# Optimization experiments

Measured on AMD Instinct MI355X. Metric: run time of the kernel, lower is better.

The kernel has to match this reference:

```python
import jax, jax.numpy as jnp
import numpy as np

N, T, F, ND, D = 64, 96, 32, 8, 128


def setup_inputs() -> dict:
    key = jax.random.key(0)
    ks = jax.random.split(key, 12)
    x = jax.random.normal(ks[0], (N, T, F), jnp.float32)
    # Wq/Wk/Wv are an (N_dim,T,D) base tiled F times -> (F*N_dim, T, D)
    Wq = jnp.tile(jax.random.normal(ks[1], (ND, T, D), jnp.float32), (F, 1, 1))
    Wk = jnp.tile(jax.random.normal(ks[2], (ND, T, D), jnp.float32), (F, 1, 1))
    Wv = jnp.tile(jax.random.normal(ks[3], (ND, T, D), jnp.float32), (F, 1, 1))
    bq = jnp.zeros((F * ND, 1, D), jnp.float32)
    bk = jnp.zeros((F * ND, 1, D), jnp.float32)
    bv = jnp.zeros((F * ND, 1, D), jnp.float32)
    # torch nn.Linear weights are (out, in); kaiming fan_in std = sqrt(2/fan_in)
    fan1 = ND * N * N
    w1 = jax.random.normal(ks[4], (ND, fan1), jnp.float32) * np.sqrt(2.0 / fan1)
    b1 = jax.random.uniform(ks[5], (ND,), jnp.float32, -0.01, 0.01)
    w2 = jax.random.normal(ks[6], (1, ND), jnp.float32) * np.sqrt(2.0 / ND)
    b2 = jax.random.uniform(ks[7], (1,), jnp.float32, -0.01, 0.01)
    w3 = jax.random.normal(ks[8], (D, D * ND), jnp.float32) * np.sqrt(2.0 / (D * ND))
    b3 = jax.random.uniform(ks[9], (D,), jnp.float32, -0.01, 0.01)
    w4 = jax.random.normal(ks[10], (T, D), jnp.float32) * np.sqrt(2.0 / D)
    b4 = jax.random.uniform(ks[11], (T,), jnp.float32, -0.01, 0.01)
    return {"x": x, "Wq": Wq, "Wk": Wk, "Wv": Wv, "bq": bq, "bk": bk, "bv": bv,
            "w1": w1, "b1": b1, "w2": w2, "b2": b2, "w3": w3, "b3": b3,
            "w4": w4, "b4": b4, "N_dim": ND}


def reference(x, Wq, Wk, Wv, bq, bk, bv, w1, b1, w2, b2, w3, b3, w4, b4, N_dim):
    n, t, f = x.shape
    d = Wq.shape[2]
    nd = N_dim
    xp = jnp.transpose(x, (2, 0, 1))                       # (F, N, T)
    # expand over heads and flatten to batched matmul: (F*N_dim, N, T)
    mat_a = jnp.broadcast_to(xp[:, None, :, :], (f, nd, n, t)).reshape(f * nd, n, t)
    q = jnp.einsum('bnt,btd->bnd', mat_a, Wq) + bq         # (F*ND, N, D)
    k = jnp.einsum('bnt,btd->bnd', mat_a, Wk) + bk
    v = jnp.einsum('bnt,btd->bnd', mat_a, Wv) + bv
    q_ = q.reshape(f, nd, n, d)
    k_ = k.reshape(f, nd, n, d)
    v_ = v.reshape(f, nd, n, d)
    # pairwise feature-feature QK^T without materializing the expanded copies
    alpha = jnp.einsum('fknd,gkmd->fgknm', q_, k_) * (d ** -0.5)  # (F,F,ND,N,N)
    alpha = alpha.reshape(f, f, nd * n * n)
    # dropout layers are identity in eval mode
    h = jax.nn.relu(alpha @ w1.T + b1)                     # (F, F, ND)
    logits = (h @ w2.T + b2)[..., 0]                       # (F, F)
    att_score = jax.nn.softmax(logits, axis=1)
    b = jnp.einsum('ij,jklm->iklm', att_score, v_)         # (F, ND, N, D)
    b = jnp.transpose(b, (0, 2, 3, 1)).reshape(f, n, d * nd)
    y = jax.nn.relu(b @ w3.T + b3)                         # (F, N, D)
    y = y @ w4.T + b4                                      # (F, N, T)
    return jnp.transpose(y, (1, 2, 0)), att_score          # (N, T, F), (F, F)
```

## Files before the change

### kernel.cpp

```cpp
#include <hip/hip_runtime.h>

#define SQKD 0.08838834764831845f

typedef __attribute__((ext_vector_type(8))) short short8;
typedef __attribute__((ext_vector_type(4))) float f32x4;

__device__ __forceinline__ unsigned short rne_bf16(float f) {
    unsigned u = __float_as_uint(f);
    return (unsigned short)((u + 0x7FFFu + ((u >> 16) & 1u)) >> 16);
}
__device__ __forceinline__ void bf16split(float f, unsigned short& hi, unsigned short& lo) {
    hi = rne_bf16(f);
    float fl = f - __uint_as_float(((unsigned)hi) << 16);
    lo = rne_bf16(fl);
}

__global__ __launch_bounds__(256) void k_prep(
    const float* __restrict__ x, const float* __restrict__ Wq,
    const float* __restrict__ Wk,
    const float* __restrict__ w1, const float* __restrict__ w3,
    unsigned short* __restrict__ Ahi, unsigned short* __restrict__ Alo,
    unsigned short* __restrict__ Wth, unsigned short* __restrict__ Wtl,
    unsigned short* __restrict__ w1h, unsigned short* __restrict__ w1l,
    unsigned short* __restrict__ w3q)
{
    __shared__ float s_ws[96 * 129];
    const int tid = threadIdx.x;
    const int bid = blockIdx.x;
    if (bid < 64) {
        const int n = bid;
        for (int e = tid; e < 3072; e += 256)
            s_ws[(e >> 5) * 33 + (e & 31)] = x[n * 3072 + e];
        __syncthreads();
        for (int o = tid; o < 3072; o += 256) {
            const int f = o / 96, t = o - f * 96;
            float v = s_ws[t * 33 + f];
            unsigned short h, l; bf16split(v, h, l);
            Ahi[f * 6144 + n * 96 + t] = h;
            Alo[f * 6144 + n * 96 + t] = l;
        }
    } else if (bid < 80) {
        const int w = bid - 64;
        const int sel = w >> 3;
        const int kh = w & 7;
        const float* src = (sel == 0 ? Wq : Wk) + kh * 12288;
        for (int e = tid; e < 12288; e += 256)
            s_ws[(e >> 7) * 129 + (e & 127)] = src[e];
        __syncthreads();
        const float sc = (sel == 0) ? SQKD : 1.0f;
        for (int o = tid; o < 12288; o += 256) {
            const int d = o / 96, t = o - d * 96;
            float v = s_ws[t * 129 + d] * sc;
            unsigned short h, l; bf16split(v, h, l);
            Wth[w * 12288 + o] = h;
            Wtl[w * 12288 + o] = l;
        }
    } else if (bid < 112) {
        const int base = (bid - 80) * 8192;
#pragma unroll
        for (int it = 0; it < 32; ++it) {
            const int i = base + it * 256 + tid;
            unsigned short h, l; bf16split(w1[i], h, l);
            w1h[i] = h; w1l[i] = l;
        }
    } else {
        const int base = (bid - 112) * 8192;
#pragma unroll
        for (int it = 0; it < 32; ++it) {
            const int o = base + it * 256 + tid;
            const int dout = o >> 10, kk = o & 1023;
            const int kh = kk >> 7, d = kk & 127;
            w3q[o] = rne_bf16(w3[dout * 1024 + d * 8 + kh]);
        }
    }
}

__global__ __launch_bounds__(256) void k_wz(
    const float* __restrict__ Wv, const float* __restrict__ bv,
    const unsigned short* __restrict__ w3q,
    unsigned short* __restrict__ WZth, unsigned short* __restrict__ WZtl,
    float* __restrict__ bzc)
{
    __shared__ __align__(16) unsigned short sB[128 * 136];
    __shared__ __align__(16) unsigned short sA2[32 * 136];
    const int tid = threadIdx.x;
    const int lane = tid & 63, wid = tid >> 6;
    const int quad = lane >> 4, col = lane & 15;
    const int bid = blockIdx.x;

    if (bid < 2) {
        f32x4 acc[6];
#pragma unroll
        for (int nt = 0; nt < 6; ++nt)
#pragma unroll
            for (int r = 0; r < 4; ++r) acc[nt][r] = 0.f;

        for (int kh = 0; kh < 8; ++kh) {
            __syncthreads();
#pragma unroll
            for (int it = 0; it < 6; ++it) {
                const int idx = it * 256 + tid;
                const int t = idx >> 4, c = idx & 15;
                const float* src = Wv + kh * 12288 + t * 128 + c * 8;
                short8 v;
#pragma unroll
                for (int j = 0; j < 8; ++j) v[j] = (short)rne_bf16(src[j]);
                *(short8*)(sB + t * 136 + c * 8) = v;
            }
            __syncthreads();
#pragma unroll
            for (int ks = 0; ks < 4; ++ks) {
                const int dout = bid * 64 + wid * 16 + col;
                short8 a = *(const short8*)(w3q + dout * 1024 + kh * 128 + ks * 32 + quad * 8);
#pragma unroll
                for (int nt = 0; nt < 6; ++nt) {
                    short8 b = *(const short8*)(sB + (nt * 16 + col) * 136 + ks * 32 + quad * 8);
                    acc[nt] = __builtin_amdgcn_mfma_f32_16x16x32_bf16(a, b, acc[nt], 0, 0, 0);
                }
            }
        }
#pragma unroll
        for (int nt = 0; nt < 6; ++nt)
#pragma unroll
            for (int r = 0; r < 4; ++r) {
                const int dout = bid * 64 + wid * 16 + quad * 4 + r;
                const int t = nt * 16 + col;
                unsigned short h, l; bf16split(acc[nt][r], h, l);
                WZth[dout * 96 + t] = h;
                WZtl[dout * 96 + t] = l;
            }
    } else {
        f32x4 acc[2][2];
#pragma unroll
        for (int mt = 0; mt < 2; ++mt)
#pragma unroll
            for (int nt = 0; nt < 2; ++nt)
#pragma unroll
                for (int r = 0; r < 4; ++r) acc[mt][nt][r] = 0.f;

        for (int kh = 0; kh < 8; ++kh) {
            __syncthreads();
#pragma unroll
            for (int it = 0; it < 2; ++it) {
                const int idx = it * 256 + tid;
                const int j = idx >> 4, c = idx & 15;
                const float* src = bv + (j * 8 + kh) * 128 + c * 8;
                short8 v;
#pragma unroll
                for (int jj = 0; jj < 8; ++jj) v[jj] = (short)rne_bf16(src[jj]);
                *(short8*)(sA2 + j * 136 + c * 8) = v;
            }
#pragma unroll
            for (int it = 0; it < 8; ++it) {
                const int idx = it * 256 + tid;
                const int dd = idx >> 4, c = idx & 15;
                *(short8*)(sB + dd * 136 + c * 8) =
                    *(const short8*)(w3q + dd * 1024 + kh * 128 + c * 8);
            }
            __syncthreads();
#pragma unroll
            for (int ks = 0; ks < 4; ++ks) {
                short8 a[2], b[2];
#pragma unroll
                for (int mt = 0; mt < 2; ++mt)
                    a[mt] = *(const short8*)(sA2 + (mt * 16 + col) * 136 + ks * 32 + quad * 8);
#pragma unroll
                for (int nt = 0; nt < 2; ++nt)
                    b[nt] = *(const short8*)(sB + ((wid * 2 + nt) * 16 + col) * 136 + ks * 32 + quad * 8);
#pragma unroll
                for (int mt = 0; mt < 2; ++mt)
#pragma unroll
                    for (int nt = 0; nt < 2; ++nt)
                        acc[mt][nt] = __builtin_amdgcn_mfma_f32_16x16x32_bf16(a[mt], b[nt], acc[mt][nt], 0, 0, 0);
            }
        }
#pragma unroll
        for (int mt = 0; mt < 2; ++mt)
#pragma unroll
            for (int nt = 0; nt < 2; ++nt)
#pragma unroll
                for (int r = 0; r < 4; ++r) {
                    const int j = mt * 16 + quad * 4 + r;
                    const int dout = (wid * 2 + nt) * 16 + col;
                    bzc[j * 128 + dout] = acc[mt][nt][r];
                }
    }
}

__global__ __launch_bounds__(256) void k_qkvg(
    const unsigned short* __restrict__ Ahi, const unsigned short* __restrict__ Alo,
    const unsigned short* __restrict__ Wth, const unsigned short* __restrict__ Wtl,
    const unsigned short* __restrict__ WZth, const unsigned short* __restrict__ WZtl,
    const float* __restrict__ bq, const float* __restrict__ bk,
    const float* __restrict__ bzc,
    unsigned short* __restrict__ qhi, unsigned short* __restrict__ qlo,
    unsigned short* __restrict__ ktH, unsigned short* __restrict__ ktL,
    float* __restrict__ Z)
{
    __shared__ __align__(16) char smem[49152];
    unsigned short* sAh = (unsigned short*)smem;
    unsigned short* sAl = (unsigned short*)(smem + 12288);
    unsigned short* sBh = (unsigned short*)(smem + 24576);
    unsigned short* sBl = (unsigned short*)(smem + 36864);
    float* Lt = (float*)smem;

    const int tid = threadIdx.x;
    const int fb = blockIdx.x, nh = blockIdx.y, b24 = blockIdx.z;
    const int sel = (b24 < 8) ? 0 : (b24 < 16) ? 1 : 2;
    const int kh = b24 & 7;

    const unsigned short* gAh = Ahi + fb * 6144;
    const unsigned short* gAl = Alo + fb * 6144;
    const unsigned short* gBh = (sel == 2) ? (WZth + nh * 64 * 96)
                                           : (Wth + (b24 * 128 + nh * 64) * 96);
    const unsigned short* gBl = (sel == 2) ? (WZtl + nh * 64 * 96)
                                           : (Wtl + (b24 * 128 + nh * 64) * 96);
#pragma unroll
    for (int it = 0; it < 3; ++it) {
        const int off = (it * 256 + tid) * 8;
        *(short8*)(sAh + off) = *(const short8*)(gAh + off);
        *(short8*)(sAl + off) = *(const short8*)(gAl + off);
        *(short8*)(sBh + off) = *(const short8*)(gBh + off);
        *(short8*)(sBl + off) = *(const short8*)(gBl + off);
    }
    __syncthreads();

    const int lane = tid & 63, wid = tid >> 6;
    const int quad = lane >> 4, col = lane & 15;
    f32x4 acc[4];
#pragma unroll
    for (int nt = 0; nt < 4; ++nt)
#pragma unroll
        for (int r = 0; r < 4; ++r) acc[nt][r] = 0.f;

#pragma unroll
    for (int ks = 0; ks < 3; ++ks) {
        const int ko = ks * 32 + quad * 8;
        short8 ah = *(const short8*)(sAh + (wid * 16 + col) * 96 + ko);
        short8 al = *(const short8*)(sAl + (wid * 16 + col) * 96 + ko);
#pragma unroll
        for (int nt = 0; nt < 4; ++nt) {
            short8 bh = *(const short8*)(sBh + (nt * 16 + col) * 96 + ko);
            short8 bl = *(const short8*)(sBl + (nt * 16 + col) * 96 + ko);
            acc[nt] = __builtin_amdgcn_mfma_f32_16x16x32_bf16(ah, bh, acc[nt], 0, 0, 0);
            acc[nt] = __builtin_amdgcn_mfma_f32_16x16x32_bf16(al, bh, acc[nt], 0, 0, 0);
            acc[nt] = __builtin_amdgcn_mfma_f32_16x16x32_bf16(ah, bl, acc[nt], 0, 0, 0);
        }
    }

    const int b = fb * 8 + kh;
    __syncthreads();
#pragma unroll
    for (int nt = 0; nt < 4; ++nt) {
        const int dl = nt * 16 + col;
        float bb = 0.f;
        if (sel == 0)      bb = bq[b * 128 + nh * 64 + dl] * SQKD;
        else if (sel == 1) bb = bk[b * 128 + nh * 64 + dl];
#pragma unroll
        for (int r = 0; r < 4; ++r)
            Lt[(wid * 16 + quad * 4 + r) * 65 + dl] = acc[nt][r] + bb;
    }
    __syncthreads();

    if (sel == 1) {
        const int dd = tid >> 2, mg = (tid & 3) * 16;
        short8 h0, h1, l0, l1;
#pragma unroll
        for (int j = 0; j < 8; ++j) {
            unsigned short h, l;
            bf16split(Lt[(mg + j) * 65 + dd], h, l);
            h0[j] = (short)h; l0[j] = (short)l;
        }
#pragma unroll
        for (int j = 0; j < 8; ++j) {
            unsigned short h, l;
            bf16split(Lt[(mg + 8 + j) * 65 + dd], h, l);
            h1[j] = (short)h; l1[j] = (short)l;
        }
        const long base = ((long)b * 128 + nh * 64 + dd) * 64 + mg;
        *(short8*)(ktH + base) = h0; *(short8*)(ktH + base + 8) = h1;
        *(short8*)(ktL + base) = l0; *(short8*)(ktL + base + 8) = l1;
    } else if (sel == 0) {
        const int n = tid >> 2, dg = (tid & 3) * 16;
        const int o = (b * 64 + n) * 128 + nh * 64 + dg;
        short8 h0, h1, l0, l1;
#pragma unroll
        for (int j = 0; j < 8; ++j) {
            unsigned short h, l;
            bf16split(Lt[n * 65 + dg + j], h, l);
            h0[j] = (short)h; l0[j] = (short)l;
        }
#pragma unroll
        for (int j = 0; j < 8; ++j) {
            unsigned short h, l;
            bf16split(Lt[n * 65 + dg + 8 + j], h, l);
            h1[j] = (short)h; l1[j] = (short)l;
        }
        *(short8*)(qhi + o) = h0; *(short8*)(qhi + o + 8) = h1;
        *(short8*)(qlo + o) = l0; *(short8*)(qlo + o + 8) = l1;
    } else {
        const int n = tid >> 2, dg = (tid & 3) * 16;
        float* Zr = Z + (fb * 64 + n) * 128 + nh * 64 + dg;
        const float* bz = bzc + fb * 128 + nh * 64 + dg;
#pragma unroll
        for (int q4 = 0; q4 < 4; ++q4) {
            f32x4 v;
            v.x = Lt[n * 65 + dg + q4 * 4 + 0] + bz[q4 * 4 + 0];
            v.y = Lt[n * 65 + dg + q4 * 4 + 1] + bz[q4 * 4 + 1];
            v.z = Lt[n * 65 + dg + q4 * 4 + 2] + bz[q4 * 4 + 2];
            v.w = Lt[n * 65 + dg + q4 * 4 + 3] + bz[q4 * 4 + 3];
            *(f32x4*)(Zr + q4 * 4) = v;
        }
    }
}

__global__ __launch_bounds__(256) void k_t(
    const unsigned short* __restrict__ ktH, const unsigned short* __restrict__ ktL,
    const unsigned short* __restrict__ w1h, const unsigned short* __restrict__ w1l,
    unsigned short* __restrict__ Tb)
{
    __shared__ __align__(16) unsigned short sH[128 * 72];
    __shared__ __align__(16) unsigned short sL[128 * 72];
    const int tid = threadIdx.x;
    const int g = blockIdx.x >> 3, kh = blockIdx.x & 7;
    const int pass = blockIdx.y;
    const int lane = tid & 63, wid = tid >> 6;
    const int quad = lane >> 4, col = lane & 15;

    {
        const unsigned short* gH = ktH + (long)(g * 8 + kh) * 8192;
        const unsigned short* gL = ktL + (long)(g * 8 + kh) * 8192;
#pragma unroll
        for (int it = 0; it < 4; ++it) {
            const int idx = it * 256 + tid;
            const int d = idx >> 3, gr = idx & 7;
            *(short8*)(sH + d * 72 + gr * 8) = *(const short8*)(gH + idx * 8);
            *(short8*)(sL + d * 72 + gr * 8) = *(const short8*)(gL + idx * 8);
        }
    }
    __syncthreads();

    const int e = wid * 2 + pass;
    f32x4 acc[4][8];
#pragma unroll
    for (int mt = 0; mt < 4; ++mt)
#pragma unroll
        for (int nt = 0; nt < 8; ++nt)
#pragma unroll
            for (int r = 0; r < 4; ++r) acc[mt][nt][r] = 0.f;

    const unsigned short* w1he = w1h + e * 32768 + kh * 4096;
    const unsigned short* w1le = w1l + e * 32768 + kh * 4096;
#pragma unroll
    for (int ks = 0; ks < 2; ++ks) {
        short8 ah[4], al[4];
#pragma unroll
        for (int mt = 0; mt < 4; ++mt) {
            const int off = (mt * 16 + col) * 64 + ks * 32 + quad * 8;
            ah[mt] = *(const short8*)(w1he + off);
            al[mt] = *(const short8*)(w1le + off);
        }
#pragma unroll
        for (int nt = 0; nt < 8; ++nt) {
            const int off = (nt * 16 + col) * 72 + ks * 32 + quad * 8;
            short8 bh = *(const short8*)(sH + off);
            short8 bl = *(const short8*)(sL + off);
#pragma unroll
            for (int mt = 0; mt < 4; ++mt) {
                acc[mt][nt] = __builtin_amdgcn_mfma_f32_16x16x32_bf16(ah[mt], bh, acc[mt][nt], 0, 0, 0);
                acc[mt][nt] = __builtin_amdgcn_mfma_f32_16x16x32_bf16(al[mt], bh, acc[mt][nt], 0, 0, 0);
                acc[mt][nt] = __builtin_amdgcn_mfma_f32_16x16x32_bf16(ah[mt], bl, acc[mt][nt], 0, 0, 0);
            }
        }
    }

    unsigned short* To = Tb + (long)(g * 8 + e) * 65536 + kh * 8192;
#pragma unroll
    for (int mt = 0; mt < 4; ++mt)
#pragma unroll
        for (int nt = 0; nt < 8; ++nt)
#pragma unroll
            for (int r = 0; r < 4; ++r) {
                const int n = mt * 16 + quad * 4 + r;
                const int d = nt * 16 + col;
                To[n * 128 + d] = rne_bf16(acc[mt][nt][r]);
            }
}

__global__ __launch_bounds__(512) void k_he(
    const unsigned short* __restrict__ Tb,
    const unsigned short* __restrict__ qhi, const unsigned short* __restrict__ qlo,
    float* __restrict__ P)
{
    const int tid = threadIdx.x;
    const int s = blockIdx.x;
    const long K0 = (long)s * 256;
    const int lane = tid & 63, wid = tid >> 6;
    const int quad = lane >> 4, col = lane & 15;

    f32x4 acc[2][2];
#pragma unroll
    for (int mt = 0; mt < 2; ++mt)
#pragma unroll
        for (int nt = 0; nt < 2; ++nt)
#pragma unroll
            for (int r = 0; r < 4; ++r) acc[mt][nt][r] = 0.f;

    for (int ks = 0; ks < 8; ++ks) {
        const long ko = K0 + ks * 32 + quad * 8;
        short8 t[2];
#pragma unroll
        for (int mt = 0; mt < 2; ++mt) {
            const int ge = (wid * 2 + mt) * 16 + col;
            t[mt] = *(const short8*)(Tb + (long)ge * 65536 + ko);
        }
#pragma unroll
        for (int nt = 0; nt < 2; ++nt) {
            const int f = nt * 16 + col;
            short8 qh = *(const short8*)(qhi + (long)f * 65536 + ko);
            short8 ql = *(const short8*)(qlo + (long)f * 65536 + ko);
#pragma unroll
            for (int mt = 0; mt < 2; ++mt) {
                acc[mt][nt] = __builtin_amdgcn_mfma_f32_16x16x32_bf16(t[mt], qh, acc[mt][nt], 0, 0, 0);
                acc[mt][nt] = __builtin_amdgcn_mfma_f32_16x16x32_bf16(t[mt], ql, acc[mt][nt], 0, 0, 0);
            }
        }
    }

    float* Pb = P + s * 8192;
#pragma unroll
    for (int mt = 0; mt < 2; ++mt)
#pragma unroll
        for (int nt = 0; nt < 2; ++nt)
#pragma unroll
            for (int r = 0; r < 4; ++r) {
                const int ge = (wid * 2 + mt) * 16 + quad * 4 + r;
                const int f = nt * 16 + col;
                Pb[ge * 32 + f] = acc[mt][nt][r];
            }
}

__global__ __launch_bounds__(256) void k_hred(const float* __restrict__ P,
                                              float* __restrict__ He)
{
    __shared__ float r[256];
    const int b = blockIdx.x;
    const int tid = threadIdx.x;
    const int li = tid & 31, s0 = tid >> 5;
    const int i = b * 32 + li;
    float a0 = 0.f, a1 = 0.f, a2 = 0.f, a3 = 0.f;
    for (int k = 0; k < 32; k += 4) {
        a0 += P[(s0 + (k + 0) * 8) * 8192 + i];
        a1 += P[(s0 + (k + 1) * 8) * 8192 + i];
        a2 += P[(s0 + (k + 2) * 8) * 8192 + i];
        a3 += P[(s0 + (k + 3) * 8) * 8192 + i];
    }
    r[s0 * 32 + li] = (a0 + a1) + (a2 + a3);
    __syncthreads();
    if (tid < 32) {
        float s = 0.f;
#pragma unroll
        for (int q = 0; q < 8; ++q) s += r[q * 32 + tid];
        He[b * 32 + tid] = s;
    }
}

__global__ __launch_bounds__(256) void k_y(
    const float* __restrict__ Z, const float* __restrict__ He,
    const float* __restrict__ b1, const float* __restrict__ w2,
    const float* __restrict__ b2, const float* __restrict__ b3,
    const float* __restrict__ w4, const float* __restrict__ b4,
    float* __restrict__ out, float* __restrict__ attOut)
{
    __shared__ __align__(16) float Zs[32 * 128];
    __shared__ float atts[1024];
    __shared__ __align__(16) float y1s[32 * 132];
    __shared__ __align__(16) float w4s[48 * 132];
    const int n = blockIdx.x;
    const int t0 = blockIdx.y * 48;
    const int tid = threadIdx.x;

#pragma unroll
    for (int it = 0; it < 4; ++it) {
        const int gdx = it * 256 + tid;
        const int j = gdx >> 5, c = gdx & 31;
        *(f32x4*)(Zs + j * 128 + c * 4) = *(const f32x4*)(Z + j * 8192 + n * 128 + c * 4);
    }
#pragma unroll
    for (int it = 0; it < 6; ++it) {
        const int gdx = it * 256 + tid;
        const int row = gdx >> 5, c = gdx & 31;
        *(f32x4*)(w4s + row * 132 + c * 4) = *(const f32x4*)(w4 + (t0 + row) * 128 + c * 4);
    }
    float* lgs = y1s;
#pragma unroll
    for (int it = 0; it < 4; ++it) {
        const int idx = it * 256 + tid;
        const int f = idx & 31, g = idx >> 5;
        float s = b2[0];
#pragma unroll
        for (int e = 0; e < 8; ++e)
            s += fmaxf(He[g * 256 + e * 32 + f] + b1[e], 0.f) * w2[e];
        lgs[f * 32 + g] = s;
    }
    __syncthreads();
    {
        const int f8 = tid >> 5, g = tid & 31;
#pragma unroll
        for (int fi = 0; fi < 4; ++fi) {
            const int f = f8 * 4 + fi;
            float s = lgs[f * 32 + g];
            float mx = s;
#pragma unroll
            for (int m = 16; m >= 1; m >>= 1) mx = fmaxf(mx, __shfl_xor(mx, m));
            float ex = expf(s - mx);
            float sum = ex;
#pragma unroll
            for (int m = 16; m >= 1; m >>= 1) sum += __shfl_xor(sum, m);
            atts[f * 32 + g] = ex / sum;
        }
    }
    __syncthreads();
    if (blockIdx.x == 0 && blockIdx.y == 0) {
#pragma unroll
        for (int it = 0; it < 4; ++it) {
            const int idx = it * 256 + tid;
            attOut[idx] = atts[idx];
        }
    }

    {
        const int ff = tid >> 3, l8 = tid & 7;
        f32x4 a4[4];
#pragma unroll
        for (int v = 0; v < 4; ++v) a4[v] = *(const f32x4*)(b3 + l8 * 16 + v * 4);
        for (int j = 0; j < 32; ++j) {
            const float a = atts[ff * 32 + j];
#pragma unroll
            for (int v = 0; v < 4; ++v) {
                f32x4 z = *(const f32x4*)(Zs + j * 128 + l8 * 16 + v * 4);
                a4[v].x += a * z.x; a4[v].y += a * z.y;
                a4[v].z += a * z.z; a4[v].w += a * z.w;
            }
        }
        __syncthreads();
#pragma unroll
        for (int v = 0; v < 4; ++v) {
            f32x4 r;
            r.x = fmaxf(a4[v].x, 0.f); r.y = fmaxf(a4[v].y, 0.f);
            r.z = fmaxf(a4[v].z, 0.f); r.w = fmaxf(a4[v].w, 0.f);
            *(f32x4*)(y1s + ff * 132 + l8 * 16 + v * 4) = r;
        }
    }
    __syncthreads();

#pragma unroll
    for (int it = 0; it < 6; ++it) {
        const int o = it * 256 + tid;
        const int tl = o >> 5, ff = o & 31;
        float s = b4[t0 + tl];
        const float* w4r = w4s + tl * 132;
        const float* y1r = y1s + ff * 132;
#pragma unroll 8
        for (int d4 = 0; d4 < 32; ++d4) {
            f32x4 w = *(const f32x4*)(w4r + d4 * 4);
            f32x4 y = *(const f32x4*)(y1r + d4 * 4);
            s += y.x * w.x + y.y * w.y + y.z * w.z + y.w * w.w;
        }
        out[n * 3072 + (t0 + tl) * 32 + ff] = s;
    }
}

extern "C" void kernel_launch(void* const* d_in, const int* in_sizes, int n_in,
                              void* d_out, int out_size, void* d_ws, size_t ws_size,
                              hipStream_t stream)
{
    const float* x  = (const float*)d_in[0];
    const float* Wq = (const float*)d_in[1];
    const float* Wk = (const float*)d_in[2];
    const float* Wv = (const float*)d_in[3];
    const float* bq = (const float*)d_in[4];
    const float* bk = (const float*)d_in[5];
    const float* bv = (const float*)d_in[6];
    const float* w1 = (const float*)d_in[7];
    const float* b1 = (const float*)d_in[8];
    const float* w2 = (const float*)d_in[9];
    const float* b2 = (const float*)d_in[10];
    const float* w3 = (const float*)d_in[11];
    const float* b3 = (const float*)d_in[12];
    const float* w4 = (const float*)d_in[13];
    const float* b4 = (const float*)d_in[14];

    float* out = (float*)d_out;
    char*  wb  = (char*)d_ws;
    unsigned short* qhi  = (unsigned short*)(wb + 0x0000000);
    unsigned short* qlo  = (unsigned short*)(wb + 0x0400000);
    unsigned short* ktH  = (unsigned short*)(wb + 0x0800000);
    unsigned short* ktL  = (unsigned short*)(wb + 0x0C00000);
    unsigned short* Tb   = (unsigned short*)(wb + 0x1000000);
    float*          Pp   = (float*)        (wb + 0x3000000);
    float*          He   = (float*)        (wb + 0x3800000);
    unsigned short* Ahi  = (unsigned short*)(wb + 0x3810000);
    unsigned short* Alo  = (unsigned short*)(wb + 0x3870000);
    unsigned short* Wth  = (unsigned short*)(wb + 0x38D0000);
    unsigned short* Wtl  = (unsigned short*)(wb + 0x3930000);
    unsigned short* w1h  = (unsigned short*)(wb + 0x3990000);
    unsigned short* w1l  = (unsigned short*)(wb + 0x3A10000);
    unsigned short* w3q  = (unsigned short*)(wb + 0x3A90000);
    unsigned short* WZth = (unsigned short*)(wb + 0x3AD0000);
    unsigned short* WZtl = (unsigned short*)(wb + 0x3AD8000);
    float*          bzc  = (float*)        (wb + 0x3AE0000);
    float*          Zb   = (float*)        (wb + 0x3AF0000);
    float* att = out + 196608;

    k_prep <<<128, 256, 0, stream>>>(x, Wq, Wk, w1, w3,
                                     Ahi, Alo, Wth, Wtl, w1h, w1l, w3q);
    k_wz   <<<3, 256, 0, stream>>>(Wv, bv, w3q, WZth, WZtl, bzc);
    k_qkvg <<<dim3(32, 2, 17), 256, 0, stream>>>(Ahi, Alo, Wth, Wtl, WZth, WZtl,
                                                 bq, bk, bzc, qhi, qlo, ktH, ktL, Zb);
    k_t    <<<dim3(256, 2), 256, 0, stream>>>(ktH, ktL, w1h, w1l, Tb);
    k_he   <<<256, 512, 0, stream>>>(Tb, qhi, qlo, Pp);
    k_hred <<<256, 256, 0, stream>>>(Pp, He);
    k_y    <<<dim3(64, 2), 256, 0, stream>>>(Zb, He, b1, w2, b2, b3, w4, b4, out, att);
}
```

Measured before the change: 178.2 us.

## Replace partial-sum reduction kernel with atomics and widen small kernel grids

k_he now atomically accumulates its partial products directly into He, which k_t zeroes beforehand, so the separate k_hred launch and the large partial buffer are removed. The k_wz weight-fold kernel is split across more blocks, with each wave taking a K slice and the slices summed through shared memory. k_y is also split into four time chunks instead of two to raise parallelism. In exchange the code pays atomic contention, gives up deterministic summation order, and loads the Z tile redundantly in more k_y blocks.

```diff
diff --git a/kernel.cpp b/kernel.cpp
--- a/kernel.cpp
+++ b/kernel.cpp
@@ -81,14 +81,16 @@
     unsigned short* __restrict__ WZth, unsigned short* __restrict__ WZtl,
     float* __restrict__ bzc)
 {
-    __shared__ __align__(16) unsigned short sB[128 * 136];
-    __shared__ __align__(16) unsigned short sA2[32 * 136];
+    __shared__ __align__(16) char smem[51200];
     const int tid = threadIdx.x;
     const int lane = tid & 63, wid = tid >> 6;
     const int quad = lane >> 4, col = lane & 15;
     const int bid = blockIdx.x;
 
-    if (bid < 2) {
+    if (bid < 8) {
+        unsigned short* usB = (unsigned short*)smem;
+        float* red = (float*)(smem + 26624);
+        const int dout0 = bid * 16;
         f32x4 acc[6];
 #pragma unroll
         for (int nt = 0; nt < 6; ++nt)
@@ -105,31 +107,34 @@
                 short8 v;
 #pragma unroll
                 for (int j = 0; j < 8; ++j) v[j] = (short)rne_bf16(src[j]);
-                *(short8*)(sB + t * 136 + c * 8) = v;
+                *(short8*)(usB + t * 136 + c * 8) = v;
             }
             __syncthreads();
-#pragma unroll
-            for (int ks = 0; ks < 4; ++ks) {
-                const int dout = bid * 64 + wid * 16 + col;
-                short8 a = *(const short8*)(w3q + dout * 1024 + kh * 128 + ks * 32 + quad * 8);
-#pragma unroll
-                for (int nt = 0; nt < 6; ++nt) {
-                    short8 b = *(const short8*)(sB + (nt * 16 + col) * 136 + ks * 32 + quad * 8);
-                    acc[nt] = __builtin_amdgcn_mfma_f32_16x16x32_bf16(a, b, acc[nt], 0, 0, 0);
-                }
+            short8 a = *(const short8*)(w3q + (dout0 + col) * 1024 + kh * 128 + wid * 32 + quad * 8);
+#pragma unroll
+            for (int nt = 0; nt < 6; ++nt) {
+                short8 b = *(const short8*)(usB + (nt * 16 + col) * 136 + wid * 32 + quad * 8);
+                acc[nt] = __builtin_amdgcn_mfma_f32_16x16x32_bf16(a, b, acc[nt], 0, 0, 0);
             }
         }
 #pragma unroll
         for (int nt = 0; nt < 6; ++nt)
 #pragma unroll
-            for (int r = 0; r < 4; ++r) {
-                const int dout = bid * 64 + wid * 16 + quad * 4 + r;
-                const int t = nt * 16 + col;
-                unsigned short h, l; bf16split(acc[nt][r], h, l);
-                WZth[dout * 96 + t] = h;
-                WZtl[dout * 96 + t] = l;
-            }
+            for (int r = 0; r < 4; ++r)
+                red[wid * 1536 + (quad * 4 + r) * 96 + nt * 16 + col] = acc[nt][r];
+        __syncthreads();
+#pragma unroll
+        for (int it = 0; it < 6; ++it) {
+            const int el = it * 256 + tid;
+            float s = red[el] + red[1536 + el] + red[3072 + el] + red[4608 + el];
+            const int dl = el / 96, t = el - dl * 96;
+            unsigned short h, l; bf16split(s, h, l);
+            WZth[(dout0 + dl) * 96 + t] = h;
+            WZtl[(dout0 + dl) * 96 + t] = l;
+        }
     } else {
+        unsigned short* sB  = (unsigned short*)smem;
+        unsigned short* sA2 = (unsigned short*)(smem + 34816);
         f32x4 acc[2][2];
 #pragma unroll
         for (int mt = 0; mt < 2; ++mt)
@@ -317,7 +322,7 @@
 __global__ __launch_bounds__(256) void k_t(
     const unsigned short* __restrict__ ktH, const unsigned short* __restrict__ ktL,
     const unsigned short* __restrict__ w1h, const unsigned short* __restrict__ w1l,
-    unsigned short* __restrict__ Tb)
+    unsigned short* __restrict__ Tb, float* __restrict__ He)
 {
     __shared__ __align__(16) unsigned short sH[128 * 72];
     __shared__ __align__(16) unsigned short sL[128 * 72];
@@ -327,6 +332,11 @@
     const int lane = tid & 63, wid = tid >> 6;
     const int quad = lane >> 4, col = lane & 15;
 
+    if (blockIdx.x == 0 && blockIdx.y == 0) {
+#pragma unroll
+        for (int i = 0; i < 32; ++i) He[i * 256 + tid] = 0.f;
+    }
+
     {
         const unsigned short* gH = ktH + (long)(g * 8 + kh) * 8192;
         const unsigned short* gL = ktL + (long)(g * 8 + kh) * 8192;
@@ -390,7 +400,7 @@
 __global__ __launch_bounds__(512) void k_he(
     const unsigned short* __restrict__ Tb,
     const unsigned short* __restrict__ qhi, const unsigned short* __restrict__ qlo,
-    float* __restrict__ P)
+    float* __restrict__ He)
 {
     const int tid = threadIdx.x;
     const int s = blockIdx.x;
@@ -427,7 +437,6 @@
         }
     }
 
-    float* Pb = P + s * 8192;
 #pragma unroll
     for (int mt = 0; mt < 2; ++mt)
 #pragma unroll
@@ -436,33 +445,8 @@
             for (int r = 0; r < 4; ++r) {
                 const int ge = (wid * 2 + mt) * 16 + quad * 4 + r;
                 const int f = nt * 16 + col;
-                Pb[ge * 32 + f] = acc[mt][nt][r];
-            }
-}
-
-__global__ __launch_bounds__(256) void k_hred(const float* __restrict__ P,
-                                              float* __restrict__ He)
-{
-    __shared__ float r[256];
-    const int b = blockIdx.x;
-    const int tid = threadIdx.x;
-    const int li = tid & 31, s0 = tid >> 5;
-    const int i = b * 32 + li;
-    float a0 = 0.f, a1 = 0.f, a2 = 0.f, a3 = 0.f;
-    for (int k = 0; k < 32; k += 4) {
-        a0 += P[(s0 + (k + 0) * 8) * 8192 + i];
-        a1 += P[(s0 + (k + 1) * 8) * 8192 + i];
-        a2 += P[(s0 + (k + 2) * 8) * 8192 + i];
-        a3 += P[(s0 + (k + 3) * 8) * 8192 + i];
-    }
-    r[s0 * 32 + li] = (a0 + a1) + (a2 + a3);
-    __syncthreads();
-    if (tid < 32) {
-        float s = 0.f;
-#pragma unroll
-        for (int q = 0; q < 8; ++q) s += r[q * 32 + tid];
-        He[b * 32 + tid] = s;
-    }
+                atomicAdd(&He[ge * 32 + f], acc[mt][nt][r]);
+            }
 }
 
 __global__ __launch_bounds__(256) void k_y(
@@ -475,9 +459,9 @@
     __shared__ __align__(16) float Zs[32 * 128];
     __shared__ float atts[1024];
     __shared__ __align__(16) float y1s[32 * 132];
-    __shared__ __align__(16) float w4s[48 * 132];
+    __shared__ __align__(16) float w4s[24 * 132];
     const int n = blockIdx.x;
-    const int t0 = blockIdx.y * 48;
+    const int t0 = blockIdx.y * 24;
     const int tid = threadIdx.x;
 
 #pragma unroll
@@ -487,7 +471,7 @@
         *(f32x4*)(Zs + j * 128 + c * 4) = *(const f32x4*)(Z + j * 8192 + n * 128 + c * 4);
     }
 #pragma unroll
-    for (int it = 0; it < 6; ++it) {
+    for (int it = 0; it < 3; ++it) {
         const int gdx = it * 256 + tid;
         const int row = gdx >> 5, c = gdx & 31;
         *(f32x4*)(w4s + row * 132 + c * 4) = *(const f32x4*)(w4 + (t0 + row) * 128 + c * 4);
@@ -555,7 +539,7 @@
     __syncthreads();
 
 #pragma unroll
-    for (int it = 0; it < 6; ++it) {
+    for (int it = 0; it < 3; ++it) {
         const int o = it * 256 + tid;
         const int tl = o >> 5, ff = o & 31;
         float s = b4[t0 + tl];
@@ -598,28 +582,26 @@
     unsigned short* ktH  = (unsigned short*)(wb + 0x0800000);
     unsigned short* ktL  = (unsigned short*)(wb + 0x0C00000);
     unsigned short* Tb   = (unsigned short*)(wb + 0x1000000);
-    float*          Pp   = (float*)        (wb + 0x3000000);
-    float*          He   = (float*)        (wb + 0x3800000);
-    unsigned short* Ahi  = (unsigned short*)(wb + 0x3810000);
-    unsigned short* Alo  = (unsigned short*)(wb + 0x3870000);
-    unsigned short* Wth  = (unsigned short*)(wb + 0x38D0000);
-    unsigned short* Wtl  = (unsigned short*)(wb + 0x3930000);
-    unsigned short* w1h  = (unsigned short*)(wb + 0x3990000);
-    unsigned short* w1l  = (unsigned short*)(wb + 0x3A10000);
-    unsigned short* w3q  = (unsigned short*)(wb + 0x3A90000);
-    unsigned short* WZth = (unsigned short*)(wb + 0x3AD0000);
-    unsigned short* WZtl = (unsigned short*)(wb + 0x3AD8000);
-    float*          bzc  = (float*)        (wb + 0x3AE0000);
-    float*          Zb   = (float*)        (wb + 0x3AF0000);
+    float*          He   = (float*)        (wb + 0x3000000);
+    unsigned short* Ahi  = (unsigned short*)(wb + 0x3010000);
+    unsigned short* Alo  = (unsigned short*)(wb + 0x3070000);
+    unsigned short* Wth  = (unsigned short*)(wb + 0x30D0000);
+    unsigned short* Wtl  = (unsigned short*)(wb + 0x3130000);
+    unsigned short* w1h  = (unsigned short*)(wb + 0x3190000);
+    unsigned short* w1l  = (unsigned short*)(wb + 0x3210000);
+    unsigned short* w3q  = (unsigned short*)(wb + 0x3290000);
+    unsigned short* WZth = (unsigned short*)(wb + 0x32D0000);
+    unsigned short* WZtl = (unsigned short*)(wb + 0x32D8000);
+    float*          bzc  = (float*)        (wb + 0x32E0000);
+    float*          Zb   = (float*)        (wb + 0x32F0000);
     float* att = out + 196608;
 
     k_prep <<<128, 256, 0, stream>>>(x, Wq, Wk, w1, w3,
                                      Ahi, Alo, Wth, Wtl, w1h, w1l, w3q);
-    k_wz   <<<3, 256, 0, stream>>>(Wv, bv, w3q, WZth, WZtl, bzc);
+    k_wz   <<<9, 256, 0, stream>>>(Wv, bv, w3q, WZth, WZtl, bzc);
     k_qkvg <<<dim3(32, 2, 17), 256, 0, stream>>>(Ahi, Alo, Wth, Wtl, WZth, WZtl,
                                                  bq, bk, bzc, qhi, qlo, ktH, ktL, Zb);
-    k_t    <<<dim3(256, 2), 256, 0, stream>>>(ktH, ktL, w1h, w1l, Tb);
-    k_he   <<<256, 512, 0, stream>>>(Tb, qhi, qlo, Pp);
-    k_hred <<<256, 256, 0, stream>>>(Pp, He);
-    k_y    <<<dim3(64, 2), 256, 0, stream>>>(Zb, He, b1, w2, b2, b3, w4, b4, out, att);
-}
+    k_t    <<<dim3(256, 2), 256, 0, stream>>>(ktH, ktL, w1h, w1l, Tb, He);
+    k_he   <<<256, 512, 0, stream>>>(Tb, qhi, qlo, He);
+    k_y    <<<dim3(64, 4), 256, 0, stream>>>(Zb, He, b1, w2, b2, b3, w4, b4, out, att);
+}
```

After: 182.2 us. +2.2%, slower.
